# Performance work log

Measured on AMD Instinct MI355X. Metric: run time of the kernel, lower is better.

Reference implementation:

```python
import jax, jax.numpy as jnp
import numpy as np

NUM_EXPERTS = 8
TOP_K = 2
BALANCE_LOSS_COEF = 0.01


def setup_inputs() -> dict:
    key = jax.random.key(0)
    ks = jax.random.split(key, 5)
    B, S, H, I, E = 8, 2048, 512, 2048, NUM_EXPERTS
    return {
        "hidden_states": jax.random.normal(ks[0], (B, S, H), dtype=jnp.float32),
        "Wg": jax.random.normal(ks[1], (H, E), dtype=jnp.float32) * (1.0 / np.sqrt(H)),
        "bg": jnp.zeros((E,), dtype=jnp.float32),
        "W1": jax.random.normal(ks[2], (E, H, I), dtype=jnp.float32) * (1.0 / np.sqrt(H)),
        "b1": jnp.zeros((E, I), dtype=jnp.float32),
        "W2": jax.random.normal(ks[3], (E, I, H), dtype=jnp.float32) * (1.0 / np.sqrt(I)),
        "b2": jnp.zeros((E, H), dtype=jnp.float32),
    }


def reference(hidden_states, Wg, bg, W1, b1, W2, b2):
    B, S, H = hidden_states.shape
    E, K = NUM_EXPERTS, TOP_K

    # ---- Router: softmax gate + top-k, renormalized weights ----
    logits = jnp.einsum('bsh,he->bse', hidden_states, Wg) + bg       # [B,S,E]
    probs = jax.nn.softmax(logits, axis=-1)                          # [B,S,E]
    top_p, top_i = jax.lax.top_k(probs, K)                           # [B,S,K]
    routing_weights = top_p / jnp.sum(top_p, axis=-1, keepdims=True)  # [B,S,K]

    # ---- Experts: compute every expert densely (small fixed E), then gather ----
    h = jnp.einsum('bsh,ehi->ebsi', hidden_states, W1) + b1[:, None, None, :]
    h = jax.nn.gelu(h)
    y = jnp.einsum('ebsi,eih->ebsh', h, W2) + b2[:, None, None, :]   # [E,B,S,H]

    y = jnp.moveaxis(y, 0, 2)                                        # [B,S,E,H]
    sel = jnp.take_along_axis(y, top_i[..., None], axis=2)           # [B,S,K,H]
    output = jnp.sum(routing_weights[..., None] * sel, axis=2) + hidden_states

    # ---- Load balancing loss (Switch-style): E * sum_e f_e * P_e ----
    assign = jnp.sum(jax.nn.one_hot(top_i, E, dtype=probs.dtype), axis=2)  # [B,S,E]
    f = jnp.mean(assign, axis=(0, 1)) / K                            # fraction dispatched
    P = jnp.mean(probs, axis=(0, 1))                                 # mean router prob
    balance_loss = BALANCE_LOSS_COEF * E * jnp.sum(f * P)

    return output, balance_loss
```

## Files before the change

kernel.cpp:

```cpp
#include <hip/hip_runtime.h>

#define BS_TOK 16384
#define HD 512
#define IDIM 2048
#define NE 8
#define RT_MAX 264
#define CAP (RT_MAX * 128)

typedef unsigned short u16;
typedef unsigned int u32;
typedef __attribute__((ext_vector_type(8))) __bf16 bf16x8;
typedef __attribute__((ext_vector_type(4))) float f32x4;

__device__ __forceinline__ u16 f2bf(float f) {
  u32 u = __builtin_bit_cast(u32, f);
  u += 0x7fffu + ((u >> 16) & 1u);
  return (u16)(u >> 16);
}
__device__ __forceinline__ float bflo(u32 u) { return __builtin_bit_cast(float, u << 16); }
__device__ __forceinline__ float bfhi(u32 u) { return __builtin_bit_cast(float, u & 0xffff0000u); }
__device__ __forceinline__ float gelu_t(float v) {
  float c = 0.7978845608028654f * (v + 0.044715f * v * v * v);
  return v / (1.0f + __expf(-2.0f * c));
}
__device__ __forceinline__ void gload16(const u16* g, u16* l) {
  __builtin_amdgcn_global_load_lds((const __attribute__((address_space(1))) u16*)g,
                                   (__attribute__((address_space(3))) u16*)l, 16, 0, 0);
}

__global__ void k_init(u32* counts, u32* pos, float* Psum, int* perm_t, float* perm_w) {
  int i = blockIdx.x * 256 + threadIdx.x;
  if (i < NE) { counts[i] = 0; pos[i] = 0; Psum[i] = 0.f; }
  if (i < CAP) { perm_t[i] = 0; perm_w[i] = 0.f; }
}

__global__ void k_transpose2(const float* __restrict__ W1, u16* __restrict__ W1T,
                             const float* __restrict__ W2, u16* __restrict__ W2T) {
  __shared__ float t[32][33];
  int z = blockIdx.z;
  const float* in; u16* out; int R, C, bx, by;
  if (z < NE) { in = W1; out = W1T; R = HD; C = IDIM; bx = blockIdx.x; by = blockIdx.y; }
  else { in = W2; out = W2T; R = IDIM; C = HD; bx = blockIdx.y; by = blockIdx.x; z -= NE; }
  size_t eb = (size_t)z * HD * IDIM;
  int c0 = bx * 32, r0 = by * 32;
  int tx = threadIdx.x, ty = threadIdx.y;
  #pragma unroll
  for (int j = ty; j < 32; j += 8) t[j][tx] = in[eb + (size_t)(r0 + j) * C + (c0 + tx)];
  __syncthreads();
  #pragma unroll
  for (int j = ty; j < 32; j += 8) out[eb + (size_t)(c0 + j) * R + (r0 + tx)] = f2bf(t[tx][j]);
}

__global__ void k_router(const float* __restrict__ x, const float* __restrict__ Wg,
                         const float* __restrict__ bg, int* __restrict__ top_e,
                         float* __restrict__ top_w, u32* __restrict__ counts,
                         float* __restrict__ Psum, u16* __restrict__ xb) {
  __shared__ float wg_s[HD * NE];
  __shared__ float Pp[NE];
  __shared__ u32 cnt[NE];
  int tid = threadIdx.x;
  if (tid < NE) { Pp[tid] = 0.f; cnt[tid] = 0; }
  for (int i = tid; i < HD * NE; i += 256) wg_s[i] = Wg[i];
  __syncthreads();
  int wv = tid >> 6, lane = tid & 63;
  int t = blockIdx.x * 4 + wv;
  const float4* xr = (const float4*)(x + (size_t)t * HD + lane * 8);
  float4 a = xr[0], b = xr[1];
  u32 p0 = f2bf(a.x) | ((u32)f2bf(a.y) << 16);
  u32 p1 = f2bf(a.z) | ((u32)f2bf(a.w) << 16);
  u32 p2 = f2bf(b.x) | ((u32)f2bf(b.y) << 16);
  u32 p3 = f2bf(b.z) | ((u32)f2bf(b.w) << 16);
  ((uint4*)(xb + (size_t)t * HD))[lane] = make_uint4(p0, p1, p2, p3);

  float acc[NE];
  #pragma unroll
  for (int e = 0; e < NE; ++e) acc[e] = 0.f;
  #pragma unroll
  for (int j = 0; j < 8; ++j) {
    float xv = j < 4 ? (&a.x)[j] : (&b.x)[j - 4];
    int h = lane * 8 + j;
    #pragma unroll
    for (int e = 0; e < NE; ++e) acc[e] += xv * wg_s[h * NE + e];
  }
  #pragma unroll
  for (int off = 32; off > 0; off >>= 1) {
    #pragma unroll
    for (int e = 0; e < NE; ++e) acc[e] += __shfl_down(acc[e], off);
  }
  if (lane == 0) {
    float lg[NE];
    #pragma unroll
    for (int e = 0; e < NE; ++e) lg[e] = acc[e] + bg[e];
    int i1 = 0; float m1 = lg[0];
    #pragma unroll
    for (int e = 1; e < NE; ++e) if (lg[e] > m1) { m1 = lg[e]; i1 = e; }
    int i2 = -1; float m2 = -1e30f;
    #pragma unroll
    for (int e = 0; e < NE; ++e) if (e != i1 && lg[e] > m2) { m2 = lg[e]; i2 = e; }
    float s = 0.f, p[NE];
    #pragma unroll
    for (int e = 0; e < NE; ++e) { p[e] = __expf(lg[e] - m1); s += p[e]; }
    float inv = 1.f / s;
    #pragma unroll
    for (int e = 0; e < NE; ++e) { p[e] *= inv; atomicAdd(&Pp[e], p[e]); }
    float denom = p[i1] + p[i2];
    top_e[2 * t] = i1; top_e[2 * t + 1] = i2;
    top_w[2 * t] = p[i1] / denom; top_w[2 * t + 1] = p[i2] / denom;
    atomicAdd(&cnt[i1], 1u); atomicAdd(&cnt[i2], 1u);
  }
  __syncthreads();
  if (tid < NE) { atomicAdd(&counts[tid], cnt[tid]); atomicAdd(&Psum[tid], Pp[tid]); }
}

__global__ void k_scan(const u32* __restrict__ counts, const float* __restrict__ Psum,
                       u32* __restrict__ padoff, u32* __restrict__ pos, float* __restrict__ out) {
  if (threadIdx.x == 0) {
    u32 off = 0; float loss = 0.f;
    for (int e = 0; e < NE; ++e) {
      padoff[e] = off; pos[e] = off;
      off += ((counts[e] + 127u) / 128u) * 128u;
      loss += ((float)counts[e] / (float)(BS_TOK * 2)) * (Psum[e] / (float)BS_TOK);
    }
    padoff[NE] = off;
    out[(size_t)BS_TOK * HD] = 0.01f * (float)NE * loss;
  }
}

__global__ void k_scatter(const int* __restrict__ top_e, const float* __restrict__ top_w,
                          u32* __restrict__ pos, int* __restrict__ perm_t,
                          float* __restrict__ perm_w, int* __restrict__ inv) {
  int g = blockIdx.x * 256 + threadIdx.x;
  int e = top_e[g]; float wgt = top_w[g];
  int lane = threadIdx.x & 63;
  #pragma unroll
  for (int ee = 0; ee < NE; ++ee) {
    unsigned long long m = __ballot(e == ee);
    if (e == ee) {
      int nb = __popcll(m & ((1ull << lane) - 1ull));
      int leader = __ffsll((unsigned long long)m) - 1;
      u32 base = 0;
      if (lane == leader) base = atomicAdd(&pos[ee], (u32)__popcll(m));
      base = __shfl(base, leader);
      int slot = (int)base + nb;
      perm_t[slot] = g >> 1;
      perm_w[slot] = wgt;
      inv[g] = slot;
    }
  }
}

__global__ void k_outinit(const float* __restrict__ x, float* __restrict__ out) {
  size_t i = (size_t)blockIdx.x * 256 + threadIdx.x;
  ((float4*)out)[i] = ((const float4*)x)[i];
}

template <int KSTEPS, int NCT, int NTOT, bool GATHER, bool ACT, bool ATOMIC>
__global__ __launch_bounds__(256, 2) void k_gemm(
    const u16* __restrict__ A, int lda, const u16* __restrict__ W,
    const float* __restrict__ bias, const int* __restrict__ perm_t,
    const float* __restrict__ perm_w, const u32* __restrict__ padoff,
    u16* __restrict__ C, float* __restrict__ outA, int rt0) {
  __shared__ u16 As[2][8192], Bs[2][8192];
  int nb = gridDim.x;
  int b = blockIdx.x;
  int tile = (b & 7) * (nb >> 3) + (b >> 3);
  int rt = rt0 + tile / NCT, ct = tile % NCT;
  u32 s0 = (u32)rt * 128u;
  if (rt >= RT_MAX || s0 >= padoff[NE]) return;
  int e = 0;
  #pragma unroll
  for (int k = 1; k < NE; ++k) e += (s0 >= padoff[k]) ? 1 : 0;

  int tid = threadIdx.x;
  int wv = tid >> 6, lane = tid & 63;
  int l15 = lane & 15, lg4 = lane >> 4;
  int wr = wv >> 1, wc = wv & 1;

  int srow = tid >> 3;
  int cb = (tid & 7) * 16;
  int cbs = (cb ^ ((srow & 7) << 4)) >> 1;

  const u16* ap[4]; const u16* bp[4];
  #pragma unroll
  for (int i = 0; i < 4; ++i) {
    int r = i * 32 + srow;
    int arow = GATHER ? perm_t[s0 + r] : (int)(s0 + r);
    ap[i] = A + (size_t)arow * lda + cbs;
    bp[i] = W + ((size_t)e * NTOT + ct * 128 + r) * (KSTEPS * 64) + cbs;
  }

  f32x4 acc[4][4] = {};

  #pragma unroll
  for (int i = 0; i < 4; ++i) gload16(ap[i], As[0] + tid * 8 + i * 2048);
  #pragma unroll
  for (int i = 0; i < 4; ++i) gload16(bp[i], Bs[0] + tid * 8 + i * 2048);
  #pragma unroll
  for (int i = 0; i < 4; ++i) gload16(ap[i] + 64, As[1] + tid * 8 + i * 2048);
  #pragma unroll
  for (int i = 0; i < 4; ++i) gload16(bp[i] + 64, Bs[1] + tid * 8 + i * 2048);
  asm volatile("s_waitcnt vmcnt(8)" ::: "memory");
  __builtin_amdgcn_sched_barrier(0);
  __builtin_amdgcn_s_barrier();

  for (int ks = 0; ks < KSTEPS; ++ks) {
    int cur = ks & 1;
    const u16* Ab = As[cur];
    const u16* Bb = Bs[cur];
    bf16x8 af[2][4], bf[2][4];
    #pragma unroll
    for (int kk = 0; kk < 2; ++kk) {
      #pragma unroll
      for (int f = 0; f < 4; ++f) {
        int ra = wr * 64 + f * 16 + l15;
        af[kk][f] = *(const bf16x8*)((const char*)Ab +
                    (ra * 128 + ((kk * 64 + lg4 * 16) ^ ((ra & 7) << 4))));
        int rb = wc * 64 + f * 16 + l15;
        bf[kk][f] = *(const bf16x8*)((const char*)Bb +
                    (rb * 128 + ((kk * 64 + lg4 * 16) ^ ((rb & 7) << 4))));
      }
    }
    asm volatile("s_waitcnt lgkmcnt(0)" ::: "memory");
    __builtin_amdgcn_sched_barrier(0);
    __builtin_amdgcn_s_barrier();

    if (ks + 2 < KSTEPS) {
      int k0 = (ks + 2) * 64;
      #pragma unroll
      for (int i = 0; i < 4; ++i) gload16(ap[i] + k0, As[cur] + tid * 8 + i * 2048);
      #pragma unroll
      for (int i = 0; i < 4; ++i) gload16(bp[i] + k0, Bs[cur] + tid * 8 + i * 2048);
    }

    __builtin_amdgcn_s_setprio(1);
    #pragma unroll
    for (int kk = 0; kk < 2; ++kk) {
      #pragma unroll
      for (int i = 0; i < 4; ++i)
        #pragma unroll
        for (int j = 0; j < 4; ++j)
          acc[i][j] = __builtin_amdgcn_mfma_f32_16x16x32_bf16(af[kk][i], bf[kk][j], acc[i][j], 0, 0, 0);
    }
    __builtin_amdgcn_s_setprio(0);

    if (ks + 1 < KSTEPS) {
      if (ks + 2 < KSTEPS) {
        asm volatile("s_waitcnt vmcnt(8)" ::: "memory");
      } else {
        asm volatile("s_waitcnt vmcnt(0)" ::: "memory");
      }
      __builtin_amdgcn_sched_barrier(0);
      __builtin_amdgcn_s_barrier();
    }
  }

  int base_n = ct * 128 + wc * 64;
  float bv[4];
  #pragma unroll
  for (int j = 0; j < 4; ++j) bv[j] = bias[e * NTOT + base_n + j * 16 + l15];

  #pragma unroll
  for (int i = 0; i < 4; ++i) {
    u32 mrow = s0 + wr * 64 + i * 16 + lg4 * 4;
    #pragma unroll
    for (int rr = 0; rr < 4; ++rr) {
      u32 m = mrow + rr;
      if (ATOMIC) {
        int tok = perm_t[m]; float wt = perm_w[m];
        if (wt != 0.f) {
          #pragma unroll
          for (int j = 0; j < 4; ++j) {
            float v = (acc[i][j][rr] + bv[j]) * wt;
            atomicAdd(outA + (size_t)tok * HD + base_n + j * 16 + l15, v);
          }
        }
      } else {
        #pragma unroll
        for (int j = 0; j < 4; ++j) {
          float v = acc[i][j][rr] + bv[j];
          if (ACT) v = gelu_t(v);
          C[(size_t)m * NTOT + base_n + j * 16 + l15] = f2bf(v);
        }
      }
    }
  }
}

__global__ void k_final(const float* __restrict__ x, const u16* __restrict__ y,
                        const int* __restrict__ inv, const float* __restrict__ top_w,
                        float* __restrict__ out) {
  int tid = threadIdx.x;
  int t = blockIdx.x * 4 + (tid >> 6);
  int lane = tid & 63;
  int s0 = inv[2 * t], s1 = inv[2 * t + 1];
  float w0 = top_w[2 * t], w1 = top_w[2 * t + 1];
  size_t xo = (size_t)t * HD + lane * 8;
  float4 a = *(const float4*)(x + xo);
  float4 b = *(const float4*)(x + xo + 4);
  uint4 ya = *(const uint4*)(y + (size_t)s0 * HD + lane * 8);
  uint4 yb = *(const uint4*)(y + (size_t)s1 * HD + lane * 8);
  float4 o0, o1;
  o0.x = a.x + w0 * bflo(ya.x) + w1 * bflo(yb.x);
  o0.y = a.y + w0 * bfhi(ya.x) + w1 * bfhi(yb.x);
  o0.z = a.z + w0 * bflo(ya.y) + w1 * bflo(yb.y);
  o0.w = a.w + w0 * bfhi(ya.y) + w1 * bfhi(yb.y);
  o1.x = b.x + w0 * bflo(ya.z) + w1 * bflo(yb.z);
  o1.y = b.y + w0 * bfhi(ya.z) + w1 * bfhi(yb.z);
  o1.z = b.z + w0 * bflo(ya.w) + w1 * bflo(yb.w);
  o1.w = b.w + w0 * bfhi(ya.w) + w1 * bfhi(yb.w);
  *(float4*)(out + xo) = o0;
  *(float4*)(out + xo + 4) = o1;
}

extern "C" void kernel_launch(void* const* d_in, const int* in_sizes, int n_in,
                              void* d_out, int out_size, void* d_ws, size_t ws_size,
                              hipStream_t stream) {
  const float* x  = (const float*)d_in[0];
  const float* Wg = (const float*)d_in[1];
  const float* bg = (const float*)d_in[2];
  const float* W1 = (const float*)d_in[3];
  const float* b1 = (const float*)d_in[4];
  const float* W2 = (const float*)d_in[5];
  const float* b2 = (const float*)d_in[6];
  float* out = (float*)d_out;

  char* w = (char*)d_ws;
  u32* counts  = (u32*)(w + 0);
  u32* pos     = (u32*)(w + 32);
  float* Psum  = (float*)(w + 64);
  u32* padoff  = (u32*)(w + 96);
  int* top_e   = (int*)(w + 256);
  float* top_w = (float*)(w + 256 + 131072);
  int* invm    = (int*)(w + 256 + 2 * 131072);
  int* perm_t  = (int*)(w + 256 + 3 * 131072);
  float* perm_w = (float*)(w + 256 + 3 * 131072 + 135168);
  u16* xb  = (u16*)(w + 663808);
  u16* W1T = (u16*)(w + 17441024);
  u16* W2T = (u16*)(w + 34218240);
  u16* h   = (u16*)(w + 50995456);
  u16* y   = (u16*)(w + 189407488);

  bool modeA = ws_size >= 224010496ull;
  int T;
  if (modeA) {
    T = RT_MAX;
  } else {
    size_t hspace = ws_size > 50995456ull ? ws_size - 50995456ull : 0;
    T = (int)(hspace / (128ull * IDIM * 2));
    T &= ~1;
    if (T < 2) return;
    if (T > RT_MAX) T = RT_MAX;
  }

  k_init<<<(CAP + 255) / 256, 256, 0, stream>>>(counts, pos, Psum, perm_t, perm_w);
  k_transpose2<<<dim3(IDIM / 32, HD / 32, 2 * NE), dim3(32, 8), 0, stream>>>(W1, W1T, W2, W2T);
  k_router<<<BS_TOK / 4, 256, 0, stream>>>(x, Wg, bg, top_e, top_w, counts, Psum, xb);
  k_scan<<<1, 64, 0, stream>>>(counts, Psum, padoff, pos, out);
  k_scatter<<<(BS_TOK * 2) / 256, 256, 0, stream>>>(top_e, top_w, pos, perm_t, perm_w, invm);
  if (!modeA) k_outinit<<<(BS_TOK * HD / 4) / 256, 256, 0, stream>>>(x, out);

  int nch = (RT_MAX + T - 1) / T;
  for (int c = 0; c < nch; ++c) {
    int rt0 = c * T;
    u16* hadj = h - (size_t)rt0 * 128 * IDIM;
    k_gemm<8, 16, IDIM, true, true, false><<<T * 16, 256, 0, stream>>>(
        xb, HD, W1T, b1, perm_t, perm_w, padoff, hadj, nullptr, rt0);
    if (modeA) {
      k_gemm<32, 4, HD, false, false, false><<<T * 4, 256, 0, stream>>>(
          hadj, IDIM, W2T, b2, perm_t, perm_w, padoff, y, nullptr, rt0);
    } else {
      k_gemm<32, 4, HD, false, false, true><<<T * 4, 256, 0, stream>>>(
          hadj, IDIM, W2T, b2, perm_t, perm_w, padoff, nullptr, out, rt0);
    }
  }
  if (modeA) k_final<<<BS_TOK / 4, 256, 0, stream>>>(x, y, invm, top_w, out);
}
```

Before: 380.2 us.

## Stage GEMM epilogue through LDS for vectorized bf16 stores; replace init kernel with memsets

The non-atomic GEMM epilogue now writes the fp32 accumulators into a padded shared-memory tile that reuses the A/B staging buffers. It then converts them to bf16 and stores 16-byte rows coalesced, replacing the scattered 2-byte stores. The k_init kernel is replaced by two hipMemsetAsync calls over the workspace regions holding the counters and permutation arrays. The epilogue adds two block barriers and LDS traffic, and the larger shared footprint may affect occupancy at 2 blocks per CU.

```diff
diff --git a/kernel.cpp b/kernel.cpp
--- a/kernel.cpp
+++ b/kernel.cpp
@@ -26,12 +26,6 @@
 __device__ __forceinline__ void gload16(const u16* g, u16* l) {
   __builtin_amdgcn_global_load_lds((const __attribute__((address_space(1))) u16*)g,
                                    (__attribute__((address_space(3))) u16*)l, 16, 0, 0);
-}
-
-__global__ void k_init(u32* counts, u32* pos, float* Psum, int* perm_t, float* perm_w) {
-  int i = blockIdx.x * 256 + threadIdx.x;
-  if (i < NE) { counts[i] = 0; pos[i] = 0; Psum[i] = 0.f; }
-  if (i < CAP) { perm_t[i] = 0; perm_w[i] = 0.f; }
 }
 
 __global__ void k_transpose2(const float* __restrict__ W1, u16* __restrict__ W1T,
@@ -160,7 +154,13 @@
     const float* __restrict__ bias, const int* __restrict__ perm_t,
     const float* __restrict__ perm_w, const u32* __restrict__ padoff,
     u16* __restrict__ C, float* __restrict__ outA, int rt0) {
-  __shared__ u16 As[2][8192], Bs[2][8192];
+  __shared__ __align__(16) char smem[128 * 130 * 4];
+  u16* As0 = (u16*)smem;
+  u16* As1 = (u16*)(smem + 16384);
+  u16* Bs0 = (u16*)(smem + 32768);
+  u16* Bs1 = (u16*)(smem + 49152);
+  float* Es = (float*)smem;
+
   int nb = gridDim.x;
   int b = blockIdx.x;
   int tile = (b & 7) * (nb >> 3) + (b >> 3);
@@ -192,21 +192,21 @@
   f32x4 acc[4][4] = {};
 
   #pragma unroll
-  for (int i = 0; i < 4; ++i) gload16(ap[i], As[0] + tid * 8 + i * 2048);
-  #pragma unroll
-  for (int i = 0; i < 4; ++i) gload16(bp[i], Bs[0] + tid * 8 + i * 2048);
-  #pragma unroll
-  for (int i = 0; i < 4; ++i) gload16(ap[i] + 64, As[1] + tid * 8 + i * 2048);
-  #pragma unroll
-  for (int i = 0; i < 4; ++i) gload16(bp[i] + 64, Bs[1] + tid * 8 + i * 2048);
+  for (int i = 0; i < 4; ++i) gload16(ap[i], As0 + tid * 8 + i * 2048);
+  #pragma unroll
+  for (int i = 0; i < 4; ++i) gload16(bp[i], Bs0 + tid * 8 + i * 2048);
+  #pragma unroll
+  for (int i = 0; i < 4; ++i) gload16(ap[i] + 64, As1 + tid * 8 + i * 2048);
+  #pragma unroll
+  for (int i = 0; i < 4; ++i) gload16(bp[i] + 64, Bs1 + tid * 8 + i * 2048);
   asm volatile("s_waitcnt vmcnt(8)" ::: "memory");
   __builtin_amdgcn_sched_barrier(0);
   __builtin_amdgcn_s_barrier();
 
   for (int ks = 0; ks < KSTEPS; ++ks) {
     int cur = ks & 1;
-    const u16* Ab = As[cur];
-    const u16* Bb = Bs[cur];
+    const u16* Ab = cur ? As1 : As0;
+    const u16* Bb = cur ? Bs1 : Bs0;
     bf16x8 af[2][4], bf[2][4];
     #pragma unroll
     for (int kk = 0; kk < 2; ++kk) {
@@ -226,10 +226,12 @@
 
     if (ks + 2 < KSTEPS) {
       int k0 = (ks + 2) * 64;
-      #pragma unroll
-      for (int i = 0; i < 4; ++i) gload16(ap[i] + k0, As[cur] + tid * 8 + i * 2048);
-      #pragma unroll
-      for (int i = 0; i < 4; ++i) gload16(bp[i] + k0, Bs[cur] + tid * 8 + i * 2048);
+      u16* Ad = cur ? As1 : As0;
+      u16* Bd = cur ? Bs1 : Bs0;
+      #pragma unroll
+      for (int i = 0; i < 4; ++i) gload16(ap[i] + k0, Ad + tid * 8 + i * 2048);
+      #pragma unroll
+      for (int i = 0; i < 4; ++i) gload16(bp[i] + k0, Bd + tid * 8 + i * 2048);
     }
 
     __builtin_amdgcn_s_setprio(1);
@@ -259,13 +261,13 @@
   #pragma unroll
   for (int j = 0; j < 4; ++j) bv[j] = bias[e * NTOT + base_n + j * 16 + l15];
 
-  #pragma unroll
-  for (int i = 0; i < 4; ++i) {
-    u32 mrow = s0 + wr * 64 + i * 16 + lg4 * 4;
-    #pragma unroll
-    for (int rr = 0; rr < 4; ++rr) {
-      u32 m = mrow + rr;
-      if (ATOMIC) {
+  if (ATOMIC) {
+    #pragma unroll
+    for (int i = 0; i < 4; ++i) {
+      u32 mrow = s0 + wr * 64 + i * 16 + lg4 * 4;
+      #pragma unroll
+      for (int rr = 0; rr < 4; ++rr) {
+        u32 m = mrow + rr;
         int tok = perm_t[m]; float wt = perm_w[m];
         if (wt != 0.f) {
           #pragma unroll
@@ -274,14 +276,35 @@
             atomicAdd(outA + (size_t)tok * HD + base_n + j * 16 + l15, v);
           }
         }
-      } else {
+      }
+    }
+  } else {
+    __syncthreads();
+    #pragma unroll
+    for (int i = 0; i < 4; ++i) {
+      int mb = wr * 64 + i * 16 + lg4 * 4;
+      #pragma unroll
+      for (int rr = 0; rr < 4; ++rr) {
         #pragma unroll
         for (int j = 0; j < 4; ++j) {
           float v = acc[i][j][rr] + bv[j];
           if (ACT) v = gelu_t(v);
-          C[(size_t)m * NTOT + base_n + j * 16 + l15] = f2bf(v);
+          Es[(mb + rr) * 130 + wc * 64 + j * 16 + l15] = v;
         }
       }
+    }
+    __syncthreads();
+    #pragma unroll
+    for (int p = 0; p < 8; ++p) {
+      int idx = tid + p * 256;
+      int row = idx >> 4, blk = idx & 15;
+      const float* src = Es + row * 130 + blk * 8;
+      u32 o0 = (u32)f2bf(src[0]) | ((u32)f2bf(src[1]) << 16);
+      u32 o1 = (u32)f2bf(src[2]) | ((u32)f2bf(src[3]) << 16);
+      u32 o2 = (u32)f2bf(src[4]) | ((u32)f2bf(src[5]) << 16);
+      u32 o3 = (u32)f2bf(src[6]) | ((u32)f2bf(src[7]) << 16);
+      *(uint4*)(C + (size_t)(s0 + row) * NTOT + ct * 128 + blk * 8) =
+          make_uint4(o0, o1, o2, o3);
     }
   }
 }
@@ -352,7 +375,8 @@
     if (T > RT_MAX) T = RT_MAX;
   }
 
-  k_init<<<(CAP + 255) / 256, 256, 0, stream>>>(counts, pos, Psum, perm_t, perm_w);
+  hipMemsetAsync(w, 0, 256, stream);
+  hipMemsetAsync(w + 393472, 0, 270336, stream);
   k_transpose2<<<dim3(IDIM / 32, HD / 32, 2 * NE), dim3(32, 8), 0, stream>>>(W1, W1T, W2, W2T);
   k_router<<<BS_TOK / 4, 256, 0, stream>>>(x, Wg, bg, top_e, top_w, counts, Psum, xb);
   k_scan<<<1, 64, 0, stream>>>(counts, Psum, padoff, pos, out);
```

Result: no change. 384.3 us (+1.1%).
